# Performance work log

Measured on AMD Instinct MI355X. Metric: run time of the kernel, lower is better.

The kernel has to match this reference:

```python
import jax, jax.numpy as jnp
import numpy as np

NUM_EXPERTS = 8
TOP_K = 2
ENTROPY_WEIGHT = 0.1
MAX_USAGE_RATIO = 0.3


def setup_inputs() -> dict:
    key = jax.random.key(0)
    k0, k1, k2 = jax.random.split(key, 3)
    B, S, D, H, E = 4, 4096, 1024, 1024, NUM_EXPERTS
    x = jax.random.normal(k0, (B, S, D), jnp.float32)
    gate_w = jax.random.normal(k1, (D, E), jnp.float32) * (1.0 / np.sqrt(D))
    gate_b = jnp.zeros((E,), jnp.float32)
    expert_w = jax.random.normal(k2, (E, D, H), jnp.float32) * (1.0 / np.sqrt(D))
    expert_b = jnp.zeros((E, H), jnp.float32)
    return {"x": x, "gate_w": gate_w, "gate_b": gate_b,
            "expert_w": expert_w, "expert_b": expert_b}


def reference(x, gate_w, gate_b, expert_w, expert_b):
    # x: [B, S, D]; dropout omitted (eval mode / deterministic reference)
    B, S, D = x.shape
    E = gate_w.shape[1]
    H = expert_w.shape[2]
    N = B * S
    xf = x.reshape(N, D)

    gate_logits = xf @ gate_w + gate_b            # [N, E]
    gate_probs = jax.nn.softmax(gate_logits, axis=-1)
    entropy = -jnp.sum(gate_probs * jnp.log(gate_probs + 1e-10), axis=-1).mean()
    entropy_loss = ENTROPY_WEIGHT * entropy

    topk_probs, topk_idx = jax.lax.top_k(gate_probs, TOP_K)   # [N, K]
    onehot = jax.nn.one_hot(topk_idx, E, dtype=xf.dtype)       # [N, K, E]
    combine = jnp.einsum('nk,nke->ne', topk_probs, onehot)     # [N, E] gating weight per expert

    # Weighted combine of per-expert Linear outputs; loop over small fixed E.
    out = jnp.zeros((N, H), xf.dtype)
    for e in range(E):
        out = out + combine[:, e:e + 1] * (xf @ expert_w[e] + expert_b[e])

    counts = jnp.sum(onehot, axis=(0, 1))                      # [E] tokens routed per expert
    usage_ratios = counts / N
    overuse_penalty = jnp.sum(jax.nn.relu(usage_ratios - MAX_USAGE_RATIO))

    return out.reshape(B, S, H), entropy_loss + overuse_penalty
```

## Files before the change

kernel.cpp:

```cpp
#include <hip/hip_runtime.h>
#include <hip/hip_bf16.h>

typedef __bf16 bf16x8 __attribute__((ext_vector_type(8)));
typedef __bf16 bf16x4 __attribute__((ext_vector_type(4)));
typedef float  f32x4  __attribute__((ext_vector_type(4)));
typedef int    i32x4  __attribute__((ext_vector_type(4)));

#define NTOK 16384
#define DDIM 1024
#define HDIM 1024
#define CNT_STRIDE 16

#define XB_OFF   0u
#define WT_OFF   33554432u
#define IDXP_OFF 50331648u
#define PPP_OFF  50397184u
#define TPID_OFF 50528256u
#define TPP_OFF  50593792u
#define CNT_OFF  50724864u
#define CUR_OFF  50728960u
#define BASE_OFF 50733056u
#define TILT_OFF 50733312u
#define NT_OFF   50736384u
#define ENT_OFF  50736388u
#define ZERO_LEN 11536u

typedef __attribute__((address_space(1))) void gvoid_t;
typedef __attribute__((address_space(3))) void lvoid_t;

__device__ __forceinline__ void cp16(void* lds, const void* g) {
  __builtin_amdgcn_global_load_lds((gvoid_t*)g, (lvoid_t*)lds, 16, 0, 0);
}

__global__ __launch_bounds__(256) void transpose_w(const float* __restrict__ w,
                                                   __bf16* __restrict__ wT,
                                                   int* __restrict__ zero_base) {
  const int t = threadIdx.x;
  if (blockIdx.x == 0) {
    i32x4* z = (i32x4*)zero_base;
    const i32x4 zz = {0, 0, 0, 0};
    for (int i = t; i < (int)(ZERO_LEN / 16); i += 256) z[i] = zz;
  }
  const int b  = blockIdx.x;
  const int e  = b >> 8;
  const int d0 = ((b >> 4) & 15) * 64;
  const int h0 = (b & 15) * 64;
  __shared__ float tile[64][69];
  const float* base = w + ((size_t)e * DDIM + d0) * HDIM + h0;
#pragma unroll
  for (int it = 0; it < 4; ++it) {
    int dl = it * 16 + (t >> 4);
    int hl = (t & 15) * 4;
    float4 v = *(const float4*)(base + (size_t)dl * HDIM + hl);
    tile[dl][hl]     = v.x;
    tile[dl][hl + 1] = v.y;
    tile[dl][hl + 2] = v.z;
    tile[dl][hl + 3] = v.w;
  }
  __syncthreads();
  __bf16* obase = wT + ((size_t)e * HDIM + h0) * DDIM + d0;
#pragma unroll
  for (int it = 0; it < 2; ++it) {
    int hl = it * 32 + (t >> 3);
    int dl = (t & 7) * 8;
    bf16x8 bv;
#pragma unroll
    for (int i = 0; i < 8; ++i) bv[i] = (__bf16)tile[dl + i][hl];
    *(bf16x8*)(obase + (size_t)hl * DDIM + dl) = bv;
  }
}

__global__ __launch_bounds__(256) void gate_kernel(
    const float* __restrict__ x, const float* __restrict__ gw,
    const float* __restrict__ gb, __bf16* __restrict__ xb,
    int* __restrict__ tt_pid, float2* __restrict__ tt_pp,
    int* __restrict__ cnt_g, float* __restrict__ ent_g) {
  __shared__ float gwT[8 * 1024];
  __shared__ int   lcnt[64];
  __shared__ float went[4];
  const int tid = threadIdx.x, w = tid >> 6, lane = tid & 63;
  for (int i = tid; i < 64; i += 256) lcnt[i] = 0;
#pragma unroll
  for (int i = 0; i < 32; ++i) {
    int lin = i * 256 + tid;
    gwT[(lin & 7) * 1024 + (lin >> 3)] = gw[lin];
  }
  __syncthreads();
  float4 gr[4][8];
#pragma unroll
  for (int j = 0; j < 4; ++j)
#pragma unroll
    for (int e = 0; e < 8; ++e)
      gr[j][e] = *(const float4*)&gwT[e * 1024 + j * 256 + lane * 4];
  float gbr[8];
#pragma unroll
  for (int e = 0; e < 8; ++e) gbr[e] = gb[e];

  float entacc = 0.f;
  for (int t = 0; t < 4; ++t) {
    const int n = blockIdx.x * 16 + w * 4 + t;
    float acc[8] = {0.f, 0.f, 0.f, 0.f, 0.f, 0.f, 0.f, 0.f};
#pragma unroll
    for (int j = 0; j < 4; ++j) {
      float4 v = *(const float4*)(x + (size_t)n * DDIM + j * 256 + lane * 4);
      bf16x4 bv;
      bv[0] = (__bf16)v.x; bv[1] = (__bf16)v.y;
      bv[2] = (__bf16)v.z; bv[3] = (__bf16)v.w;
      *(bf16x4*)(xb + (size_t)n * DDIM + j * 256 + lane * 4) = bv;
#pragma unroll
      for (int e = 0; e < 8; ++e) {
        float4 g = gr[j][e];
        acc[e] += v.x * g.x + v.y * g.y + v.z * g.z + v.w * g.w;
      }
    }
#pragma unroll
    for (int e = 0; e < 8; ++e) {
      float s = acc[e];
#pragma unroll
      for (int off = 1; off < 64; off <<= 1) s += __shfl_xor(s, off);
      acc[e] = s;
    }
    float p[8], lg[8];
    float mx = -1e30f;
#pragma unroll
    for (int e = 0; e < 8; ++e) { p[e] = acc[e] + gbr[e]; mx = fmaxf(mx, p[e]); }
    float s = 0.f;
#pragma unroll
    for (int e = 0; e < 8; ++e) { lg[e] = p[e] - mx; p[e] = expf(lg[e]); s += p[e]; }
    float inv = 1.0f / s;
    float dot = 0.f;
#pragma unroll
    for (int e = 0; e < 8; ++e) { p[e] *= inv; dot += p[e] * lg[e]; }
    entacc += logf(s) - dot;
    int e1 = 0; float p1 = p[0];
#pragma unroll
    for (int e = 1; e < 8; ++e) if (p[e] > p1) { p1 = p[e]; e1 = e; }
    int e2 = (e1 == 0) ? 1 : 0; float p2 = p[e2];
#pragma unroll
    for (int e = 0; e < 8; ++e) if (e != e1 && p[e] > p2) { p2 = p[e]; e2 = e; }
    int   elo = (e1 < e2) ? e1 : e2;
    int   ehi = (e1 < e2) ? e2 : e1;
    float plo = (e1 < e2) ? p1 : p2;
    float phi = (e1 < e2) ? p2 : p1;
    int pid = elo * 8 + ehi;
    if (lane == 0) {
      tt_pid[n] = pid;
      tt_pp[n]  = make_float2(plo, phi);
      atomicAdd(&lcnt[pid], 1);
    }
  }
  if (lane == 0) went[w] = entacc;
  __syncthreads();
  if (tid < 64 && lcnt[tid]) atomicAdd(&cnt_g[tid * CNT_STRIDE], lcnt[tid]);
  if (tid == 0)
    atomicAdd(ent_g, went[0] + went[1] + went[2] + went[3]);
}

__global__ void scan_kernel(const int* __restrict__ cnt_g, int* __restrict__ base_g,
                            int4* __restrict__ tilt, int* __restrict__ nt_g,
                            const float* __restrict__ ent_g, float* __restrict__ loss_out) {
  __shared__ int csh[64];
  const int t = threadIdx.x;
  csh[t] = cnt_g[t * CNT_STRIDE];
  __syncthreads();
  if (t == 0) {
    int b = 0, ti = 0;
    int ecnt[8] = {0, 0, 0, 0, 0, 0, 0, 0};
    for (int pid = 0; pid < 64; ++pid) {
      int c = csh[pid];
      base_g[pid] = b;
      if (c > 0) {
        ecnt[pid >> 3] += c;
        ecnt[pid & 7]  += c;
        for (int r = 0; r < c; r += 128) tilt[ti++] = make_int4(pid, r, c, b);
        b += c;
      }
    }
    *nt_g = ti;
    float pen = 0.f;
    for (int e = 0; e < 8; ++e) {
      float r = (float)ecnt[e] / (float)NTOK - 0.3f;
      if (r > 0.f) pen += r;
    }
    loss_out[0] = 0.1f * (ent_g[0] / (float)NTOK) + pen;
  }
}

__global__ __launch_bounds__(256) void scatter_kernel(
    const int* __restrict__ tt_pid, const float2* __restrict__ tt_pp,
    const int* __restrict__ base_g, int* __restrict__ cur_g,
    int* __restrict__ idx_p, float2* __restrict__ pp_p) {
  __shared__ int lcnt[64], lbase[64];
  const int tid = threadIdx.x;
  if (tid < 64) lcnt[tid] = 0;
  __syncthreads();
  const int n = blockIdx.x * 256 + tid;
  const int pid = tt_pid[n];
  int lofs = atomicAdd(&lcnt[pid], 1);
  __syncthreads();
  if (tid < 64 && lcnt[tid]) lbase[tid] = atomicAdd(&cur_g[tid * CNT_STRIDE], lcnt[tid]);
  __syncthreads();
  int dst = base_g[pid] + lbase[pid] + lofs;
  idx_p[dst] = n;
  pp_p[dst]  = tt_pp[n];
}

__global__ __launch_bounds__(256) void moe_gemm(
    const __bf16* __restrict__ xb, const __bf16* __restrict__ wT,
    const float* __restrict__ eb, const int* __restrict__ idx_p,
    const float2* __restrict__ pp_p, const int4* __restrict__ tilt,
    const int* __restrict__ nt_g, float* __restrict__ out) {
  const int lin = blockIdx.y * 8 + blockIdx.x;
  const int gy  = (lin & 7) + 8 * (lin >> 6);
  const int gx  = (lin >> 3) & 7;
  if (gy >= *nt_g) return;
  const int4 te = tilt[gy];
  const int pid = te.x, row0 = te.y, cntp = te.z, gbase = te.w;
  const int elo = pid >> 3, ehi = pid & 7;

  __shared__ __bf16 Ash[128 * 64];
  __shared__ __bf16 BloS[128 * 64];
  __shared__ __bf16 BhiS[128 * 64];
  __shared__ int    tok_s[128];
  __shared__ float2 pp_s[128];

  const int tid = threadIdx.x, w = tid >> 6, lane = tid & 63;
  if (tid < 128) {
    int s = row0 + tid;
    int g = gbase + ((s < cntp) ? s : (cntp - 1));
    tok_s[tid] = idx_p[g];
    pp_s[tid]  = pp_p[g];
  }
  __syncthreads();

  f32x4 accL[4][4], accH[4][4];
  const f32x4 zero = {0.f, 0.f, 0.f, 0.f};
#pragma unroll
  for (int mi = 0; mi < 4; ++mi)
#pragma unroll
    for (int ni = 0; ni < 4; ++ni) { accL[mi][ni] = zero; accH[mi][ni] = zero; }

  const int wm = (w >> 1) * 64, wn = (w & 1) * 64;
  const int tq = lane >> 4, tr = lane & 15, tr7 = tr & 7;
  const int rsub = lane >> 3;
  const int csw = ((lane & 7) ^ rsub) * 8;

  const __bf16* wlo = wT + (size_t)elo * HDIM * DDIM + (size_t)(gx * 128) * DDIM;
  const __bf16* whi = wT + (size_t)ehi * HDIM * DDIM + (size_t)(gx * 128) * DDIM;
  const __bf16* aptr[4];
  const __bf16* lptr[4];
  const __bf16* hptr[4];
#pragma unroll
  for (int it = 0; it < 4; ++it) {
    int r = it * 32 + w * 8 + rsub;
    aptr[it] = xb + (size_t)tok_s[r] * DDIM + csw;
    lptr[it] = wlo + (size_t)r * DDIM + csw;
    hptr[it] = whi + (size_t)r * DDIM + csw;
  }

  for (int kk = 0; kk < 16; ++kk) {
#pragma unroll
    for (int it = 0; it < 4; ++it) {
      const int rb = it * 32 + w * 8;
      cp16((char*)Ash  + rb * 128, aptr[it]); aptr[it] += 64;
      cp16((char*)BloS + rb * 128, lptr[it]); lptr[it] += 64;
      cp16((char*)BhiS + rb * 128, hptr[it]); hptr[it] += 64;
    }
    __syncthreads();
#pragma unroll
    for (int h = 0; h < 2; ++h) {
      const int co = (h << 2) | tq;
      bf16x8 a[4], bl[4], bh[4];
#pragma unroll
      for (int mi = 0; mi < 4; ++mi)
        a[mi] = *(const bf16x8*)((const char*)Ash + (wm + mi * 16 + tr) * 128 +
                                 ((co ^ tr7) << 4));
#pragma unroll
      for (int ni = 0; ni < 4; ++ni) {
        bl[ni] = *(const bf16x8*)((const char*)BloS + (wn + ni * 16 + tr) * 128 +
                                  ((co ^ tr7) << 4));
        bh[ni] = *(const bf16x8*)((const char*)BhiS + (wn + ni * 16 + tr) * 128 +
                                  ((co ^ tr7) << 4));
      }
#pragma unroll
      for (int mi = 0; mi < 4; ++mi)
#pragma unroll
        for (int ni = 0; ni < 4; ++ni) {
          accL[mi][ni] = __builtin_amdgcn_mfma_f32_16x16x32_bf16(a[mi], bl[ni], accL[mi][ni], 0, 0, 0);
          accH[mi][ni] = __builtin_amdgcn_mfma_f32_16x16x32_bf16(a[mi], bh[ni], accH[mi][ni], 0, 0, 0);
        }
    }
    __syncthreads();
  }

  float blov[4], bhiv[4];
#pragma unroll
  for (int ni = 0; ni < 4; ++ni) {
    int col = gx * 128 + wn + ni * 16 + tr;
    blov[ni] = eb[elo * HDIM + col];
    bhiv[ni] = eb[ehi * HDIM + col];
  }
#pragma unroll
  for (int mi = 0; mi < 4; ++mi)
#pragma unroll
    for (int r = 0; r < 4; ++r) {
      int lr = wm + mi * 16 + tq * 4 + r;
      if (row0 + lr < cntp) {
        int    tok = tok_s[lr];
        float2 pp  = pp_s[lr];
        float* orow = out + (size_t)tok * HDIM + gx * 128 + wn + tr;
#pragma unroll
        for (int ni = 0; ni < 4; ++ni)
          orow[ni * 16] = pp.x * (accL[mi][ni][r] + blov[ni]) +
                          pp.y * (accH[mi][ni][r] + bhiv[ni]);
      }
    }
}

extern "C" void kernel_launch(void* const* d_in, const int* in_sizes, int n_in,
                              void* d_out, int out_size, void* d_ws, size_t ws_size,
                              hipStream_t stream) {
  const float* x  = (const float*)d_in[0];
  const float* gw = (const float*)d_in[1];
  const float* gb = (const float*)d_in[2];
  const float* ew = (const float*)d_in[3];
  const float* eb = (const float*)d_in[4];
  float* out = (float*)d_out;
  char*  ws  = (char*)d_ws;

  __bf16* xb     = (__bf16*)(ws + XB_OFF);
  __bf16* wT     = (__bf16*)(ws + WT_OFF);
  int*    idx_p  = (int*)(ws + IDXP_OFF);
  float2* pp_p   = (float2*)(ws + PPP_OFF);
  int*    tt_pid = (int*)(ws + TPID_OFF);
  float2* tt_pp  = (float2*)(ws + TPP_OFF);
  int*    cnt_g  = (int*)(ws + CNT_OFF);
  int*    cur_g  = (int*)(ws + CUR_OFF);
  int*    base_g = (int*)(ws + BASE_OFF);
  int4*   tilt   = (int4*)(ws + TILT_OFF);
  int*    nt_g   = (int*)(ws + NT_OFF);
  float*  ent_g  = (float*)(ws + ENT_OFF);

  transpose_w<<<dim3(2048), 256, 0, stream>>>(ew, wT, cnt_g);
  gate_kernel<<<dim3(1024), 256, 0, stream>>>(x, gw, gb, xb, tt_pid, tt_pp,
                                              cnt_g, ent_g);
  scan_kernel<<<1, 64, 0, stream>>>(cnt_g, base_g, tilt, nt_g, ent_g,
                                    out + (size_t)NTOK * HDIM);
  scatter_kernel<<<dim3(64), 256, 0, stream>>>(tt_pid, tt_pp, base_g, cur_g,
                                               idx_p, pp_p);
  moe_gemm<<<dim3(8, 160), 256, 0, stream>>>(xb, wT, eb, idx_p, pp_p, tilt,
                                             nt_g, out);
}
```

Baseline: 323.4 us.

## Merge transpose and gate kernels, drop scan kernel and global atomics

The weight transpose and gating kernel are combined into one prep launch that splits work by block index, so the two phases can run together. Per-block pair counts and entropy partials are written to arrays instead of being accumulated with global atomics, which removes the workspace zeroing and the single-thread scan kernel. The scatter kernel now rebuilds the prefix offsets itself from those per-block counts, and each GEMM block works out its own tile header from the totals. This cuts two launches and the serial steps between them, at the cost of repeated redundant prefix scans in every scatter and GEMM block.

```diff
diff --git a/kernel.cpp b/kernel.cpp
--- a/kernel.cpp
+++ b/kernel.cpp
@@ -4,12 +4,10 @@
 typedef __bf16 bf16x8 __attribute__((ext_vector_type(8)));
 typedef __bf16 bf16x4 __attribute__((ext_vector_type(4)));
 typedef float  f32x4  __attribute__((ext_vector_type(4)));
-typedef int    i32x4  __attribute__((ext_vector_type(4)));
 
 #define NTOK 16384
 #define DDIM 1024
 #define HDIM 1024
-#define CNT_STRIDE 16
 
 #define XB_OFF   0u
 #define WT_OFF   33554432u
@@ -17,13 +15,9 @@
 #define PPP_OFF  50397184u
 #define TPID_OFF 50528256u
 #define TPP_OFF  50593792u
-#define CNT_OFF  50724864u
-#define CUR_OFF  50728960u
-#define BASE_OFF 50733056u
-#define TILT_OFF 50733312u
-#define NT_OFF   50736384u
-#define ENT_OFF  50736388u
-#define ZERO_LEN 11536u
+#define CNTB_OFF 50724864u
+#define ENTB_OFF 50790400u
+#define TOT_OFF  50794496u
 
 typedef __attribute__((address_space(1))) void gvoid_t;
 typedef __attribute__((address_space(3))) void lvoid_t;
@@ -32,53 +26,52 @@
   __builtin_amdgcn_global_load_lds((gvoid_t*)g, (lvoid_t*)lds, 16, 0, 0);
 }
 
-__global__ __launch_bounds__(256) void transpose_w(const float* __restrict__ w,
-                                                   __bf16* __restrict__ wT,
-                                                   int* __restrict__ zero_base) {
-  const int t = threadIdx.x;
-  if (blockIdx.x == 0) {
-    i32x4* z = (i32x4*)zero_base;
-    const i32x4 zz = {0, 0, 0, 0};
-    for (int i = t; i < (int)(ZERO_LEN / 16); i += 256) z[i] = zz;
-  }
-  const int b  = blockIdx.x;
-  const int e  = b >> 8;
-  const int d0 = ((b >> 4) & 15) * 64;
-  const int h0 = (b & 15) * 64;
-  __shared__ float tile[64][69];
-  const float* base = w + ((size_t)e * DDIM + d0) * HDIM + h0;
-#pragma unroll
-  for (int it = 0; it < 4; ++it) {
-    int dl = it * 16 + (t >> 4);
-    int hl = (t & 15) * 4;
-    float4 v = *(const float4*)(base + (size_t)dl * HDIM + hl);
-    tile[dl][hl]     = v.x;
-    tile[dl][hl + 1] = v.y;
-    tile[dl][hl + 2] = v.z;
-    tile[dl][hl + 3] = v.w;
-  }
-  __syncthreads();
-  __bf16* obase = wT + ((size_t)e * HDIM + h0) * DDIM + d0;
-#pragma unroll
-  for (int it = 0; it < 2; ++it) {
-    int hl = it * 32 + (t >> 3);
-    int dl = (t & 7) * 8;
-    bf16x8 bv;
-#pragma unroll
-    for (int i = 0; i < 8; ++i) bv[i] = (__bf16)tile[dl + i][hl];
-    *(bf16x8*)(obase + (size_t)hl * DDIM + dl) = bv;
-  }
-}
-
-__global__ __launch_bounds__(256) void gate_kernel(
+__global__ __launch_bounds__(256) void prep_kernel(
+    const float* __restrict__ ew, __bf16* __restrict__ wT,
     const float* __restrict__ x, const float* __restrict__ gw,
     const float* __restrict__ gb, __bf16* __restrict__ xb,
     int* __restrict__ tt_pid, float2* __restrict__ tt_pp,
-    int* __restrict__ cnt_g, float* __restrict__ ent_g) {
-  __shared__ float gwT[8 * 1024];
-  __shared__ int   lcnt[64];
-  __shared__ float went[4];
-  const int tid = threadIdx.x, w = tid >> 6, lane = tid & 63;
+    unsigned char* __restrict__ cnt_blk, float* __restrict__ ent_blk) {
+  __shared__ __align__(16) char smem[33040];
+  const int tid = threadIdx.x;
+
+  if (blockIdx.x < 2048) {
+    typedef float (*TileT)[69];
+    TileT tile = (TileT)smem;
+    const int b  = blockIdx.x;
+    const int e  = b >> 8;
+    const int d0 = ((b >> 4) & 15) * 64;
+    const int h0 = (b & 15) * 64;
+    const float* base = ew + ((size_t)e * DDIM + d0) * HDIM + h0;
+#pragma unroll
+    for (int it = 0; it < 4; ++it) {
+      int dl = it * 16 + (tid >> 4);
+      int hl = (tid & 15) * 4;
+      float4 v = *(const float4*)(base + (size_t)dl * HDIM + hl);
+      tile[dl][hl]     = v.x;
+      tile[dl][hl + 1] = v.y;
+      tile[dl][hl + 2] = v.z;
+      tile[dl][hl + 3] = v.w;
+    }
+    __syncthreads();
+    __bf16* obase = wT + ((size_t)e * HDIM + h0) * DDIM + d0;
+#pragma unroll
+    for (int it = 0; it < 2; ++it) {
+      int hl = it * 32 + (tid >> 3);
+      int dl = (tid & 7) * 8;
+      bf16x8 bv;
+#pragma unroll
+      for (int i = 0; i < 8; ++i) bv[i] = (__bf16)tile[dl + i][hl];
+      *(bf16x8*)(obase + (size_t)hl * DDIM + dl) = bv;
+    }
+    return;
+  }
+
+  float* gwT  = (float*)smem;
+  int*   lcnt = (int*)(smem + 32768);
+  float* went = (float*)(smem + 33024);
+  const int bid = blockIdx.x - 2048;
+  const int wv = tid >> 6, lane = tid & 63;
   for (int i = tid; i < 64; i += 256) lcnt[i] = 0;
 #pragma unroll
   for (int i = 0; i < 32; ++i) {
@@ -98,7 +91,7 @@
 
   float entacc = 0.f;
   for (int t = 0; t < 4; ++t) {
-    const int n = blockIdx.x * 16 + w * 4 + t;
+    const int n = bid * 16 + wv * 4 + t;
     float acc[8] = {0.f, 0.f, 0.f, 0.f, 0.f, 0.f, 0.f, 0.f};
 #pragma unroll
     for (int j = 0; j < 4; ++j) {
@@ -149,82 +142,118 @@
       atomicAdd(&lcnt[pid], 1);
     }
   }
-  if (lane == 0) went[w] = entacc;
-  __syncthreads();
-  if (tid < 64 && lcnt[tid]) atomicAdd(&cnt_g[tid * CNT_STRIDE], lcnt[tid]);
-  if (tid == 0)
-    atomicAdd(ent_g, went[0] + went[1] + went[2] + went[3]);
-}
-
-__global__ void scan_kernel(const int* __restrict__ cnt_g, int* __restrict__ base_g,
-                            int4* __restrict__ tilt, int* __restrict__ nt_g,
-                            const float* __restrict__ ent_g, float* __restrict__ loss_out) {
-  __shared__ int csh[64];
-  const int t = threadIdx.x;
-  csh[t] = cnt_g[t * CNT_STRIDE];
-  __syncthreads();
-  if (t == 0) {
-    int b = 0, ti = 0;
-    int ecnt[8] = {0, 0, 0, 0, 0, 0, 0, 0};
-    for (int pid = 0; pid < 64; ++pid) {
-      int c = csh[pid];
-      base_g[pid] = b;
-      if (c > 0) {
-        ecnt[pid >> 3] += c;
-        ecnt[pid & 7]  += c;
-        for (int r = 0; r < c; r += 128) tilt[ti++] = make_int4(pid, r, c, b);
-        b += c;
-      }
-    }
-    *nt_g = ti;
-    float pen = 0.f;
-    for (int e = 0; e < 8; ++e) {
-      float r = (float)ecnt[e] / (float)NTOK - 0.3f;
-      if (r > 0.f) pen += r;
-    }
-    loss_out[0] = 0.1f * (ent_g[0] / (float)NTOK) + pen;
-  }
+  if (lane == 0) went[wv] = entacc;
+  __syncthreads();
+  if (tid < 64) cnt_blk[bid * 64 + tid] = (unsigned char)lcnt[tid];
+  if (tid == 0) ent_blk[bid] = went[0] + went[1] + went[2] + went[3];
 }
 
 __global__ __launch_bounds__(256) void scatter_kernel(
     const int* __restrict__ tt_pid, const float2* __restrict__ tt_pp,
-    const int* __restrict__ base_g, int* __restrict__ cur_g,
-    int* __restrict__ idx_p, float2* __restrict__ pp_p) {
-  __shared__ int lcnt[64], lbase[64];
-  const int tid = threadIdx.x;
-  if (tid < 64) lcnt[tid] = 0;
-  __syncthreads();
-  const int n = blockIdx.x * 256 + tid;
+    const unsigned char* __restrict__ cnt_blk, const float* __restrict__ ent_blk,
+    int* __restrict__ idx_p, float2* __restrict__ pp_p,
+    int* __restrict__ tot_g, float* __restrict__ loss_out) {
+  __shared__ int part_tot[4][64], part_off[4][64];
+  __shared__ int tot_l[64], off_l[64], base_l[64], lcnt[64];
+  __shared__ float esum[4];
+  const int t = threadIdx.x, b = blockIdx.x;
+  const int p = t & 63, q = t >> 6;
+  const int bcut = b * 16;
+
+  int s_tot = 0, s_off = 0;
+  for (int i = 0; i < 256; ++i) {
+    int bb = q * 256 + i;
+    int c = cnt_blk[bb * 64 + p];
+    s_tot += c;
+    s_off += (bb < bcut) ? c : 0;
+  }
+  part_tot[q][p] = s_tot;
+  part_off[q][p] = s_off;
+  if (t < 64) lcnt[t] = 0;
+  __syncthreads();
+  if (t < 64) {
+    tot_l[t] = part_tot[0][t] + part_tot[1][t] + part_tot[2][t] + part_tot[3][t];
+    off_l[t] = part_off[0][t] + part_off[1][t] + part_off[2][t] + part_off[3][t];
+  }
+  __syncthreads();
+  if (t < 64) {
+    int base = 0;
+    for (int i = 0; i < t; ++i) base += tot_l[i];
+    base_l[t] = base;
+  }
+  const int n   = b * 256 + t;
   const int pid = tt_pid[n];
+  const float2 pp = tt_pp[n];
+  __syncthreads();
   int lofs = atomicAdd(&lcnt[pid], 1);
-  __syncthreads();
-  if (tid < 64 && lcnt[tid]) lbase[tid] = atomicAdd(&cur_g[tid * CNT_STRIDE], lcnt[tid]);
-  __syncthreads();
-  int dst = base_g[pid] + lbase[pid] + lofs;
+  int dst = base_l[pid] + off_l[pid] + lofs;
   idx_p[dst] = n;
-  pp_p[dst]  = tt_pp[n];
+  pp_p[dst]  = pp;
+
+  if (b == 0) {
+    if (t < 64) tot_g[t] = tot_l[t];
+    float e = ent_blk[t] + ent_blk[t + 256] + ent_blk[t + 512] + ent_blk[t + 768];
+#pragma unroll
+    for (int off = 1; off < 64; off <<= 1) e += __shfl_xor(e, off);
+    if ((t & 63) == 0) esum[t >> 6] = e;
+    __syncthreads();
+    if (t == 0) {
+      float ent = esum[0] + esum[1] + esum[2] + esum[3];
+      int ecnt[8] = {0, 0, 0, 0, 0, 0, 0, 0};
+      for (int pd = 0; pd < 64; ++pd) {
+        int c = tot_l[pd];
+        ecnt[pd >> 3] += c;
+        ecnt[pd & 7]  += c;
+      }
+      float pen = 0.f;
+      for (int e8 = 0; e8 < 8; ++e8) {
+        float r = (float)ecnt[e8] / (float)NTOK - 0.3f;
+        if (r > 0.f) pen += r;
+      }
+      loss_out[0] = 0.1f * (ent / (float)NTOK) + pen;
+    }
+  }
 }
 
 __global__ __launch_bounds__(256) void moe_gemm(
     const __bf16* __restrict__ xb, const __bf16* __restrict__ wT,
     const float* __restrict__ eb, const int* __restrict__ idx_p,
-    const float2* __restrict__ pp_p, const int4* __restrict__ tilt,
-    const int* __restrict__ nt_g, float* __restrict__ out) {
-  const int lin = blockIdx.y * 8 + blockIdx.x;
-  const int gy  = (lin & 7) + 8 * (lin >> 6);
-  const int gx  = (lin >> 3) & 7;
-  if (gy >= *nt_g) return;
-  const int4 te = tilt[gy];
-  const int pid = te.x, row0 = te.y, cntp = te.z, gbase = te.w;
-  const int elo = pid >> 3, ehi = pid & 7;
+    const float2* __restrict__ pp_p, const int* __restrict__ tot_g,
+    float* __restrict__ out) {
+  const int gy = blockIdx.y, gx = blockIdx.x;
 
   __shared__ __bf16 Ash[128 * 64];
   __shared__ __bf16 BloS[128 * 64];
   __shared__ __bf16 BhiS[128 * 64];
   __shared__ int    tok_s[128];
   __shared__ float2 pp_s[128];
+  __shared__ int    tot_s[64];
+  __shared__ int    hdr[4];
 
   const int tid = threadIdx.x, w = tid >> 6, lane = tid & 63;
+  if (tid < 64) tot_s[tid] = tot_g[tid];
+  __syncthreads();
+  if (tid == 0) {
+    int bacc = 0, ti = 0, fpid = -1, frow = 0, fcnt = 0, fbase = 0;
+    for (int pd = 0; pd < 64; ++pd) {
+      int c = tot_s[pd];
+      if (c > 0) {
+        int ntl = (c + 127) >> 7;
+        if (gy >= ti && gy < ti + ntl) {
+          fpid = pd; frow = (gy - ti) * 128; fcnt = c; fbase = bacc;
+        }
+        ti += ntl;
+        bacc += c;
+      }
+    }
+    hdr[0] = fpid; hdr[1] = frow; hdr[2] = fcnt; hdr[3] = fbase;
+  }
+  __syncthreads();
+  const int pid = hdr[0];
+  if (pid < 0) return;
+  const int row0 = hdr[1], cntp = hdr[2], gbase = hdr[3];
+  const int elo = pid >> 3, ehi = pid & 7;
+
   if (tid < 128) {
     int s = row0 + tid;
     int g = gbase + ((s < cntp) ? s : (cntp - 1));
@@ -334,20 +363,15 @@
   float2* pp_p   = (float2*)(ws + PPP_OFF);
   int*    tt_pid = (int*)(ws + TPID_OFF);
   float2* tt_pp  = (float2*)(ws + TPP_OFF);
-  int*    cnt_g  = (int*)(ws + CNT_OFF);
-  int*    cur_g  = (int*)(ws + CUR_OFF);
-  int*    base_g = (int*)(ws + BASE_OFF);
-  int4*   tilt   = (int4*)(ws + TILT_OFF);
-  int*    nt_g   = (int*)(ws + NT_OFF);
-  float*  ent_g  = (float*)(ws + ENT_OFF);
-
-  transpose_w<<<dim3(2048), 256, 0, stream>>>(ew, wT, cnt_g);
-  gate_kernel<<<dim3(1024), 256, 0, stream>>>(x, gw, gb, xb, tt_pid, tt_pp,
-                                              cnt_g, ent_g);
-  scan_kernel<<<1, 64, 0, stream>>>(cnt_g, base_g, tilt, nt_g, ent_g,
-                                    out + (size_t)NTOK * HDIM);
-  scatter_kernel<<<dim3(64), 256, 0, stream>>>(tt_pid, tt_pp, base_g, cur_g,
-                                               idx_p, pp_p);
-  moe_gemm<<<dim3(8, 160), 256, 0, stream>>>(xb, wT, eb, idx_p, pp_p, tilt,
-                                             nt_g, out);
-}
+  unsigned char* cnt_blk = (unsigned char*)(ws + CNTB_OFF);
+  float*  ent_blk = (float*)(ws + ENTB_OFF);
+  int*    tot_g   = (int*)(ws + TOT_OFF);
+
+  prep_kernel<<<dim3(3072), 256, 0, stream>>>(ew, wT, x, gw, gb, xb,
+                                              tt_pid, tt_pp, cnt_blk, ent_blk);
+  scatter_kernel<<<dim3(64), 256, 0, stream>>>(tt_pid, tt_pp, cnt_blk, ent_blk,
+                                               idx_p, pp_p, tot_g,
+                                               out + (size_t)NTOK * HDIM);
+  moe_gemm<<<dim3(8, 160), 256, 0, stream>>>(xb, wT, eb, idx_p, pp_p, tot_g,
+                                             out);
+}
```

New measurement: 331.3 us. 2.4% more time.
